# Kernel optimization log

Hardware: AMD Instinct MI355X
Metric: run time of the kernel (lower is better)

The kernel has to match this reference:

```python
import jax, jax.numpy as jnp
import numpy as np

NEG_BIG = -9e15  # matches -9000000000000000.0 in the torch source
ALPHA = 0.2      # LeakyReLU negative slope


def setup_inputs() -> dict:
    key = jax.random.key(0)
    k1, k2, k3, k4 = jax.random.split(key, 4)
    N, F_in, F_out = 8192, 256, 128
    x = jax.random.normal(k1, (N, F_in), dtype=jnp.float32)
    adj = jax.random.randint(k2, (N, N), 0, 2, dtype=jnp.int32)
    W = jax.random.normal(k3, (F_in, F_out), dtype=jnp.float32) * 0.05
    a = jax.random.normal(k4, (2 * F_out, 1), dtype=jnp.float32) * 0.05
    return {"x": x, "adj": adj, "W": W, "a": a}


def reference(x, adj, W, a):
    # h = x @ W : [N, F]
    h = x @ W
    F_out = W.shape[1]
    # Algebraically identical to the concat formulation:
    # a^T [h_i || h_j] = h_i @ a1 + h_j @ a2
    a1 = a[:F_out, 0]
    a2 = a[F_out:, 0]
    src = h @ a1  # [N]
    dst = h @ a2  # [N]
    e = jax.nn.leaky_relu(src[:, None] + dst[None, :], negative_slope=ALPHA)  # [N, N]
    attention = jnp.where(adj > 0, e, NEG_BIG)
    attention = jax.nn.softmax(attention, axis=1)
    # dropout is identity in eval mode (training=False)
    h_prime = attention @ h  # [N, F]
    return h_prime
```

## Files before the change

### kernel.cpp

```cpp
#include <hip/hip_runtime.h>
#include <cstdint>

#define N 8192
#define FIN 256
#define FOUT 128
#define ALPHA 0.2f

typedef unsigned short u16;
typedef __attribute__((ext_vector_type(8))) short short8;
typedef __attribute__((ext_vector_type(4))) float floatx4;

__device__ __forceinline__ u16 bf16_rne(float f) {
  uint32_t u = __float_as_uint(f);
  u += 0x7fff + ((u >> 16) & 1);
  return (u16)(u >> 16);
}

__device__ __forceinline__ void gl_lds16(const void* g, void* l) {
  __builtin_amdgcn_global_load_lds(
      (const __attribute__((address_space(1))) void*)g,
      (__attribute__((address_space(3))) void*)l, 16, 0, 0);
}

__global__ __launch_bounds__(256) void k_proj(const float* __restrict__ x,
                                              const float* __restrict__ W,
                                              const float* __restrict__ a,
                                              u16* __restrict__ hT3,
                                              float* __restrict__ srcv,
                                              float* __restrict__ dstv) {
  __shared__ float xs[8 * FIN];
  __shared__ float partS[4][4], partD[4][4];
  const int t = threadIdx.x;
  const int R0 = blockIdx.x * 8;

  const float4* xv = (const float4*)(x + (size_t)R0 * FIN);
  float4* xsv = (float4*)xs;
  xsv[t] = xv[t];
  xsv[t + 256] = xv[t + 256];
  __syncthreads();

  const int c  = t & 127;
  const int rg = (t >> 7) * 4;

  float acc[4] = {0.f, 0.f, 0.f, 0.f};
  float wa[4], wb[4];
  #pragma unroll
  for (int j = 0; j < 4; ++j) wa[j] = W[j * FOUT + c];
  #pragma unroll
  for (int j = 0; j < 4; ++j) wb[j] = W[(4 + j) * FOUT + c];

  for (int k4 = 0; k4 < FIN / 4; ++k4) {
    float wc[4];
    #pragma unroll
    for (int j = 0; j < 4; ++j) { wc[j] = wa[j]; wa[j] = wb[j]; }
    const int kn = (k4 + 2 < FIN / 4) ? k4 + 2 : k4;
    #pragma unroll
    for (int j = 0; j < 4; ++j) wb[j] = W[(kn * 4 + j) * FOUT + c];
    #pragma unroll
    for (int i = 0; i < 4; ++i) {
      const float4 xq = *(const float4*)&xs[(rg + i) * FIN + k4 * 4];
      acc[i] += xq.x * wc[0] + xq.y * wc[1] + xq.z * wc[2] + xq.w * wc[3];
    }
  }

  {
    const int j = R0 + rg;
    const int jb = j >> 5, q = (j >> 3) & 3, jj = j & 7;
    const int m = c & 15, nt = c >> 4;
    union { u16 u[4]; uint2 v; } pk;
    #pragma unroll
    for (int i = 0; i < 4; ++i) pk.u[i] = bf16_rne(acc[i]);
    *(uint2*)(hT3 + (size_t)(((jb * 8 + nt) * 64) + (m * 4 + q)) * 8 + jj) = pk.v;
  }

  const float a1 = a[c], a2 = a[FOUT + c];
  float s4[4], d4[4];
  #pragma unroll
  for (int i = 0; i < 4; ++i) { s4[i] = acc[i] * a1; d4[i] = acc[i] * a2; }
  #pragma unroll
  for (int off = 32; off > 0; off >>= 1) {
    #pragma unroll
    for (int i = 0; i < 4; ++i) {
      s4[i] += __shfl_down(s4[i], off);
      d4[i] += __shfl_down(d4[i], off);
    }
  }
  const int wv = t >> 6, lane = t & 63;
  if (lane == 0) {
    #pragma unroll
    for (int i = 0; i < 4; ++i) { partS[wv][i] = s4[i]; partD[wv][i] = d4[i]; }
  }
  __syncthreads();
  if (t < 16) {
    const int i = t & 3, rg2 = (t >> 2) & 1, which = t >> 3;
    if (which == 0) srcv[R0 + rg2 * 4 + i] = partS[rg2*2][i] + partS[rg2*2+1][i];
    else            dstv[R0 + rg2 * 4 + i] = partD[rg2*2][i] + partD[rg2*2+1][i];
  }
}

__global__ __launch_bounds__(256) void k_pgen(const int* __restrict__ adj,
                                              const float* __restrict__ srcv,
                                              const float* __restrict__ dstv,
                                              u16* __restrict__ Pt,
                                              float* __restrict__ lp) {
  const int t  = threadIdx.x;
  const int rb = blockIdx.x >> 1;
  const int jh = blockIdx.x & 1;
  const int R0 = rb * 16;
  const int j0 = jh * 4096;
  const int m  = t >> 4;
  const int sx = t & 15;

  const float srcr = srcv[R0 + m];
  const int*   ap = adj + (size_t)(R0 + m) * N + j0 + sx * 4;
  const float* dp = dstv + j0 + sx * 4;
  u16* pp = Pt + ((size_t)(rb * 256 + jh * 128 + (sx >> 3)) * 512)
               + m * 32 + ((sx & 7) * 4);

  float lsum = 0.f;
  #pragma unroll 4
  for (int kp = 0; kp < 64; ++kp) {
    const int4   A = *(const int4*)(ap + kp * 64);
    const float4 D = *(const float4*)(dp + kp * 64);
    const int   ai[4] = {A.x, A.y, A.z, A.w};
    const float df[4] = {D.x, D.y, D.z, D.w};
    union { u16 u[4]; uint2 v; } pk;
    #pragma unroll
    for (int e = 0; e < 4; ++e) {
      float v = srcr + df[e];
      v = fmaxf(v, ALPHA * v);
      const float p = ai[e] > 0 ? __expf(v) : 0.f;
      lsum += p;
      pk.u[e] = bf16_rne(p);
    }
    *(uint2*)(pp + (size_t)kp * 1024) = pk.v;
  }

  lsum += __shfl_xor(lsum, 1);
  lsum += __shfl_xor(lsum, 2);
  lsum += __shfl_xor(lsum, 4);
  lsum += __shfl_xor(lsum, 8);
  if (sx == 0) lp[(size_t)jh * N + R0 + m] = lsum;
}

__global__ __launch_bounds__(256, 4) void k_av(const u16* __restrict__ Pt,
                                               const u16* __restrict__ hT3,
                                               float* __restrict__ P2) {
  __shared__ u16 aS[2][4 * 512];
  __shared__ u16 bS[2][8 * 512];
  const int t = threadIdx.x, wv = t >> 6, lane = t & 63;
  const int q = lane >> 4, m = lane & 15, Lq = m * 4 + q;
  const int rb32 = blockIdx.x >> 2;
  const int ch   = (blockIdx.x >> 1) & 1;
  const int ksp  = blockIdx.x & 1;
  const int R0 = rb32 * 32;
  const int kb0 = ksp * 128;
  const int rh = wv & 1, ntp = wv >> 1;

  floatx4 acc[2];
  acc[0] = (floatx4){0.f, 0.f, 0.f, 0.f};
  acc[1] = (floatx4){0.f, 0.f, 0.f, 0.f};

  #define STAGE(I, BUF)                                                        \
  {                                                                            \
    _Pragma("unroll")                                                          \
    for (int cc = 0; cc < 3; ++cc) {                                           \
      const int d = wv * 3 + cc;                                               \
      if (d < 4) {                                                             \
        const int rr = d >> 1, kk = d & 1;                                     \
        const u16* s = Pt + ((size_t)((rb32 * 2 + rr) * 256 + kb0 + (I) * 2 + kk)) * 512 \
                       + (size_t)lane * 8;                                     \
        gl_lds16(s, &aS[BUF][d * 512]);                                        \
      } else {                                                                 \
        const int e = d - 4, jbx = e >> 2, nn = e & 3;                         \
        const u16* s = hT3 + ((size_t)(kb0 + (I) * 2 + jbx) * 8 + ch * 4 + nn) * 512 \
                       + (size_t)lane * 8;                                     \
        gl_lds16(s, &bS[BUF][e * 512]);                                        \
      }                                                                        \
    }                                                                          \
  }

  #define MFMA_TILE(BUF)                                                       \
  {                                                                            \
    _Pragma("unroll")                                                          \
    for (int kk = 0; kk < 2; ++kk) {                                           \
      const short8 af = *(const short8*)&aS[BUF][(rh * 2 + kk) * 512 + Lq * 8];\
      _Pragma("unroll")                                                        \
      for (int nn = 0; nn < 2; ++nn) {                                         \
        const short8 bf =                                                      \
            *(const short8*)&bS[BUF][(kk * 4 + ntp * 2 + nn) * 512 + Lq * 8];  \
        acc[nn] = __builtin_amdgcn_mfma_f32_16x16x32_bf16(af, bf, acc[nn], 0, 0, 0); \
      }                                                                        \
    }                                                                          \
  }

  STAGE(0, 0)
  for (int i = 0; i < 64; i += 2) {
    __syncthreads();
    { const int nx = (i + 1 < 64) ? i + 1 : i; STAGE(nx, 1) }
    MFMA_TILE(0)
    __syncthreads();
    { const int nx = (i + 2 < 64) ? i + 2 : i + 1; STAGE(nx, 0) }
    MFMA_TILE(1)
  }
  #undef STAGE
  #undef MFMA_TILE
  __syncthreads();

  float* Pp = P2 + ((size_t)ksp * N + R0 + rh * 16) * FOUT + ch * 64 + ntp * 32 + m;
  #pragma unroll
  for (int nn = 0; nn < 2; ++nn)
    #pragma unroll
    for (int ri = 0; ri < 4; ++ri)
      Pp[(size_t)(q * 4 + ri) * FOUT + nn * 16] = acc[nn][ri];
}

__global__ __launch_bounds__(256) void k_norm(const float* __restrict__ P2,
                                              const float* __restrict__ lp,
                                              float* __restrict__ out) {
  const int idx = blockIdx.x * 256 + threadIdx.x;
  const int rr = idx >> 5;
  const int c4 = (idx & 31) * 4;
  const float inv = 1.0f / (lp[rr] + lp[N + rr]);
  const float4 p0 = *(const float4*)(P2 + (size_t)rr * FOUT + c4);
  const float4 p1 = *(const float4*)(P2 + ((size_t)N + rr) * FOUT + c4);
  float4 s;
  s.x = (p0.x + p1.x) * inv;
  s.y = (p0.y + p1.y) * inv;
  s.z = (p0.z + p1.z) * inv;
  s.w = (p0.w + p1.w) * inv;
  *(float4*)(out + (size_t)rr * FOUT + c4) = s;
}

extern "C" void kernel_launch(void* const* d_in, const int* in_sizes, int n_in,
                              void* d_out, int out_size, void* d_ws, size_t ws_size,
                              hipStream_t stream) {
  const float* x   = (const float*)d_in[0];
  const int*   adj = (const int*)d_in[1];
  const float* W   = (const float*)d_in[2];
  const float* a   = (const float*)d_in[3];
  float* out = (float*)d_out;

  char* ws = (char*)d_ws;
  u16*   hT3  = (u16*)ws;     ws += (size_t)FOUT * N * sizeof(u16);
  float* srcv = (float*)ws;   ws += (size_t)N * sizeof(float);
  float* dstv = (float*)ws;   ws += (size_t)N * sizeof(float);
  u16*   Pt   = (u16*)ws;     ws += (size_t)N * N * sizeof(u16);
  float* lp   = (float*)ws;   ws += (size_t)2 * N * sizeof(float);
  float* P2   = (float*)ws;   ws += (size_t)2 * N * FOUT * sizeof(float);

  k_proj<<<N / 8, 256, 0, stream>>>(x, W, a, hT3, srcv, dstv);
  k_pgen<<<1024, 256, 0, stream>>>(adj, srcv, dstv, Pt, lp);
  k_av  <<<1024, 256, 0, stream>>>(Pt, hT3, P2);
  k_norm<<<(N * FOUT / 4) / 256, 256, 0, stream>>>(P2, lp, out);
}
```

Baseline: 472.8 us.

## Retile AV GEMM to 64-row blocks with 4-way K split; split pgen columns 4-way

The attention-value kernel now gives each block 64 rows and 64 output columns with a four-way K split instead of 32 rows and a two-way split. Each wave computes four 16x16 tiles, so every A fragment loaded from LDS is reused across more MFMAs. The probability-generation kernel is split into four column chunks with more blocks and a higher occupancy hint, and its row-block index now varies fastest across blocks. The normalization kernel sums four partial results and four partial row sums, which adds partial-buffer traffic in exchange for better reuse and parallelism.

```diff
diff --git a/kernel.cpp b/kernel.cpp
--- a/kernel.cpp
+++ b/kernel.cpp
@@ -98,28 +98,28 @@
   }
 }
 
-__global__ __launch_bounds__(256) void k_pgen(const int* __restrict__ adj,
-                                              const float* __restrict__ srcv,
-                                              const float* __restrict__ dstv,
-                                              u16* __restrict__ Pt,
-                                              float* __restrict__ lp) {
+__global__ __launch_bounds__(256, 8) void k_pgen(const int* __restrict__ adj,
+                                                 const float* __restrict__ srcv,
+                                                 const float* __restrict__ dstv,
+                                                 u16* __restrict__ Pt,
+                                                 float* __restrict__ lp) {
   const int t  = threadIdx.x;
-  const int rb = blockIdx.x >> 1;
-  const int jh = blockIdx.x & 1;
+  const int rb = blockIdx.x & 511;
+  const int js = blockIdx.x >> 9;
   const int R0 = rb * 16;
-  const int j0 = jh * 4096;
+  const int j0 = js * 2048;
   const int m  = t >> 4;
   const int sx = t & 15;
 
   const float srcr = srcv[R0 + m];
   const int*   ap = adj + (size_t)(R0 + m) * N + j0 + sx * 4;
   const float* dp = dstv + j0 + sx * 4;
-  u16* pp = Pt + ((size_t)(rb * 256 + jh * 128 + (sx >> 3)) * 512)
+  u16* pp = Pt + ((size_t)(rb * 256 + js * 64 + (sx >> 3)) * 512)
                + m * 32 + ((sx & 7) * 4);
 
   float lsum = 0.f;
-  #pragma unroll 4
-  for (int kp = 0; kp < 64; ++kp) {
+  #pragma unroll 8
+  for (int kp = 0; kp < 32; ++kp) {
     const int4   A = *(const int4*)(ap + kp * 64);
     const float4 D = *(const float4*)(dp + kp * 64);
     const int   ai[4] = {A.x, A.y, A.z, A.w};
@@ -140,40 +140,38 @@
   lsum += __shfl_xor(lsum, 2);
   lsum += __shfl_xor(lsum, 4);
   lsum += __shfl_xor(lsum, 8);
-  if (sx == 0) lp[(size_t)jh * N + R0 + m] = lsum;
+  if (sx == 0) lp[(size_t)js * N + R0 + m] = lsum;
 }
 
 __global__ __launch_bounds__(256, 4) void k_av(const u16* __restrict__ Pt,
                                                const u16* __restrict__ hT3,
-                                               float* __restrict__ P2) {
-  __shared__ u16 aS[2][4 * 512];
+                                               float* __restrict__ P4) {
+  __shared__ u16 aS[2][8 * 512];
   __shared__ u16 bS[2][8 * 512];
   const int t = threadIdx.x, wv = t >> 6, lane = t & 63;
   const int q = lane >> 4, m = lane & 15, Lq = m * 4 + q;
-  const int rb32 = blockIdx.x >> 2;
-  const int ch   = (blockIdx.x >> 1) & 1;
-  const int ksp  = blockIdx.x & 1;
-  const int R0 = rb32 * 32;
-  const int kb0 = ksp * 128;
-  const int rh = wv & 1, ntp = wv >> 1;
-
-  floatx4 acc[2];
-  acc[0] = (floatx4){0.f, 0.f, 0.f, 0.f};
-  acc[1] = (floatx4){0.f, 0.f, 0.f, 0.f};
+  const int rb64 = blockIdx.x & 127;
+  const int ch   = (blockIdx.x >> 7) & 1;
+  const int ksp  = blockIdx.x >> 8;
+  const int kb0  = ksp * 64;
+
+  floatx4 acc[4];
+  #pragma unroll
+  for (int nn = 0; nn < 4; ++nn) acc[nn] = (floatx4){0.f, 0.f, 0.f, 0.f};
 
   #define STAGE(I, BUF)                                                        \
   {                                                                            \
     _Pragma("unroll")                                                          \
-    for (int cc = 0; cc < 3; ++cc) {                                           \
-      const int d = wv * 3 + cc;                                               \
-      if (d < 4) {                                                             \
+    for (int cc = 0; cc < 4; ++cc) {                                           \
+      const int d = wv * 4 + cc;                                               \
+      if (d < 8) {                                 \
         const int rr = d >> 1, kk = d & 1;                                     \
-        const u16* s = Pt + ((size_t)((rb32 * 2 + rr) * 256 + kb0 + (I) * 2 + kk)) * 512 \
+        const u16* s = Pt + ((size_t)((rb64 * 4 + rr) * 256 + kb0 + (I) * 2 + kk)) * 512 \
                        + (size_t)lane * 8;                                     \
         gl_lds16(s, &aS[BUF][d * 512]);                                        \
-      } else {                                                                 \
-        const int e = d - 4, jbx = e >> 2, nn = e & 3;                         \
-        const u16* s = hT3 + ((size_t)(kb0 + (I) * 2 + jbx) * 8 + ch * 4 + nn) * 512 \
+      } else {                            \
+        const int e = d - 8, kk = e >> 2, nn = e & 3;                          \
+        const u16* s = hT3 + ((size_t)(kb0 + (I) * 2 + kk) * 8 + ch * 4 + nn) * 512 \
                        + (size_t)lane * 8;                                     \
         gl_lds16(s, &bS[BUF][e * 512]);                                        \
       }                                                                        \
@@ -184,51 +182,53 @@
   {                                                                            \
     _Pragma("unroll")                                                          \
     for (int kk = 0; kk < 2; ++kk) {                                           \
-      const short8 af = *(const short8*)&aS[BUF][(rh * 2 + kk) * 512 + Lq * 8];\
+      const short8 af = *(const short8*)&aS[BUF][(wv * 2 + kk) * 512 + Lq * 8];\
       _Pragma("unroll")                                                        \
-      for (int nn = 0; nn < 2; ++nn) {                                         \
+      for (int nn = 0; nn < 4; ++nn) {                                         \
         const short8 bf =                                                      \
-            *(const short8*)&bS[BUF][(kk * 4 + ntp * 2 + nn) * 512 + Lq * 8];  \
+            *(const short8*)&bS[BUF][(kk * 4 + nn) * 512 + Lq * 8];            \
         acc[nn] = __builtin_amdgcn_mfma_f32_16x16x32_bf16(af, bf, acc[nn], 0, 0, 0); \
       }                                                                        \
     }                                                                          \
   }
 
   STAGE(0, 0)
-  for (int i = 0; i < 64; i += 2) {
+  for (int i = 0; i < 32; i += 2) {
     __syncthreads();
-    { const int nx = (i + 1 < 64) ? i + 1 : i; STAGE(nx, 1) }
+    { const int nx = (i + 1 < 32) ? i + 1 : i; STAGE(nx, 1) }
     MFMA_TILE(0)
     __syncthreads();
-    { const int nx = (i + 2 < 64) ? i + 2 : i + 1; STAGE(nx, 0) }
+    { const int nx = (i + 2 < 32) ? i + 2 : i + 1; STAGE(nx, 0) }
     MFMA_TILE(1)
   }
   #undef STAGE
   #undef MFMA_TILE
-  __syncthreads();
-
-  float* Pp = P2 + ((size_t)ksp * N + R0 + rh * 16) * FOUT + ch * 64 + ntp * 32 + m;
-  #pragma unroll
-  for (int nn = 0; nn < 2; ++nn)
+
+  float* Pp = P4 + ((size_t)ksp * N + rb64 * 64 + wv * 16) * FOUT + ch * 64 + m;
+  #pragma unroll
+  for (int nn = 0; nn < 4; ++nn)
     #pragma unroll
     for (int ri = 0; ri < 4; ++ri)
       Pp[(size_t)(q * 4 + ri) * FOUT + nn * 16] = acc[nn][ri];
 }
 
-__global__ __launch_bounds__(256) void k_norm(const float* __restrict__ P2,
+__global__ __launch_bounds__(256) void k_norm(const float* __restrict__ P4,
                                               const float* __restrict__ lp,
                                               float* __restrict__ out) {
   const int idx = blockIdx.x * 256 + threadIdx.x;
   const int rr = idx >> 5;
   const int c4 = (idx & 31) * 4;
-  const float inv = 1.0f / (lp[rr] + lp[N + rr]);
-  const float4 p0 = *(const float4*)(P2 + (size_t)rr * FOUT + c4);
-  const float4 p1 = *(const float4*)(P2 + ((size_t)N + rr) * FOUT + c4);
-  float4 s;
-  s.x = (p0.x + p1.x) * inv;
-  s.y = (p0.y + p1.y) * inv;
-  s.z = (p0.z + p1.z) * inv;
-  s.w = (p0.w + p1.w) * inv;
+  float l = 0.f;
+  #pragma unroll
+  for (int s = 0; s < 4; ++s) l += lp[(size_t)s * N + rr];
+  const float inv = 1.0f / l;
+  float4 s = {0.f, 0.f, 0.f, 0.f};
+  #pragma unroll
+  for (int p = 0; p < 4; ++p) {
+    const float4 v = *(const float4*)(P4 + ((size_t)p * N + rr) * FOUT + c4);
+    s.x += v.x; s.y += v.y; s.z += v.z; s.w += v.w;
+  }
+  s.x *= inv; s.y *= inv; s.z *= inv; s.w *= inv;
   *(float4*)(out + (size_t)rr * FOUT + c4) = s;
 }
 
@@ -246,11 +246,11 @@
   float* srcv = (float*)ws;   ws += (size_t)N * sizeof(float);
   float* dstv = (float*)ws;   ws += (size_t)N * sizeof(float);
   u16*   Pt   = (u16*)ws;     ws += (size_t)N * N * sizeof(u16);
-  float* lp   = (float*)ws;   ws += (size_t)2 * N * sizeof(float);
-  float* P2   = (float*)ws;   ws += (size_t)2 * N * FOUT * sizeof(float);
+  float* lp   = (float*)ws;   ws += (size_t)4 * N * sizeof(float);
+  float* P4   = (float*)ws;   ws += (size_t)4 * N * FOUT * sizeof(float);
 
   k_proj<<<N / 8, 256, 0, stream>>>(x, W, a, hT3, srcv, dstv);
-  k_pgen<<<1024, 256, 0, stream>>>(adj, srcv, dstv, Pt, lp);
-  k_av  <<<1024, 256, 0, stream>>>(Pt, hT3, P2);
-  k_norm<<<(N * FOUT / 4) / 256, 256, 0, stream>>>(P2, lp, out);
-}
+  k_pgen<<<2048, 256, 0, stream>>>(adj, srcv, dstv, Pt, lp);
+  k_av  <<<1024, 256, 0, stream>>>(Pt, hT3, P4);
+  k_norm<<<(N * FOUT / 4) / 256, 256, 0, stream>>>(P4, lp, out);
+}
```

Result: faster. 462.9 us (-2.1%).
